# Performance work log

Hardware: AMD Instinct MI355X
Metric: run time of the kernel (lower is better)

## Reference

```python
import jax, jax.numpy as jnp
import numpy as np

N, E = 50000, 1600000
DIM_IN, HEADS, DIM_OUT = 256, 4, 32
NEG_SLOPE = 0.2


def setup_inputs() -> dict:
    key = jax.random.key(0)
    k1, k2, k3, k4, k5, k6 = jax.random.split(key, 6)
    x = jax.random.normal(k1, (N, DIM_IN), dtype=jnp.float32)
    edge_index = jax.random.randint(k2, (2, E), 0, N, dtype=jnp.int64)
    s = 1.0 / np.sqrt(DIM_IN)
    W = jax.random.normal(k3, (DIM_IN, HEADS * DIM_OUT), dtype=jnp.float32) * s
    att_src = jax.random.normal(k4, (HEADS, DIM_OUT), dtype=jnp.float32) * 0.1
    att_dst = jax.random.normal(k5, (HEADS, DIM_OUT), dtype=jnp.float32) * 0.1
    bias = jax.random.normal(k6, (HEADS * DIM_OUT,), dtype=jnp.float32) * 0.01
    return {"x": x, "edge_index": edge_index, "W": W,
            "att_src": att_src, "att_dst": att_dst, "bias": bias}


def reference(x, edge_index, W, att_src, att_dst, bias):
    n = x.shape[0]
    h, c = att_src.shape
    # linear projection, per-head view [N, H, C]
    xp = (x @ W).reshape(n, h, c)
    # per-node attention logits [N, H]
    a_src = jnp.einsum('nhc,hc->nh', xp, att_src)
    a_dst = jnp.einsum('nhc,hc->nh', xp, att_dst)
    # add self loops (PyG default add_self_loops=True)
    loops = jnp.arange(n, dtype=edge_index.dtype)
    src = jnp.concatenate([edge_index[0], loops])  # [E+N]
    dst = jnp.concatenate([edge_index[1], loops])
    # edge attention scores [E+N, H]
    e = jax.nn.leaky_relu(a_src[src] + a_dst[dst], negative_slope=NEG_SLOPE)
    # segment softmax over incoming edges of each dst node
    emax = jax.ops.segment_max(e, dst, num_segments=n)
    ex = jnp.exp(e - emax[dst])
    denom = jax.ops.segment_sum(ex, dst, num_segments=n)
    alpha = ex / denom[dst]  # [E+N, H]
    # weighted scatter-aggregate of src features
    msg = xp[src] * alpha[:, :, None]  # [E+N, H, C]
    out = jax.ops.segment_sum(msg, dst, num_segments=n)  # [N, H, C]
    return out.reshape(n, h * c) + bias
```

## Files before the change

kernel.cpp:

```cpp
#include <hip/hip_runtime.h>
#include <hip/hip_fp16.h>


#define DIN 256
#define HC 128
#define NH 4
#define NEG 0.2f
#define BCAP 12288
#define LOG2E 1.44269504f

typedef _Float16 half8 __attribute__((ext_vector_type(8)));
typedef _Float16 half2v __attribute__((ext_vector_type(2)));
typedef float f32x4 __attribute__((ext_vector_type(4)));

__device__ __forceinline__ void proj_body(char* sm, int tid, const float* __restrict__ x,
                                          const _Float16* __restrict__ Wt,
                                          const float* __restrict__ attS,
                                          const float* __restrict__ attD,
                                          __half* __restrict__ xph,
                                          float* __restrict__ a_src,
                                          float* __restrict__ a_dst, int n, int node0) {
    _Float16* xs = (_Float16*)sm;
    _Float16* Wl = (_Float16*)(sm + 5120);
    _Float16* ep = (_Float16*)sm;
    float* attSL = (float*)(sm + 17408);
    float* attDL = (float*)(sm + 17920);

    const int wave = tid >> 6;
    const int lane = tid & 63;
    const int l15  = lane & 15;
    const int quad = lane >> 4;

    if (tid < 128) attSL[tid] = attS[tid];
    else           attDL[tid - 128] = attD[tid - 128];

    f32x4 acc[8];
#pragma unroll
    for (int ct = 0; ct < 8; ++ct) acc[ct] = (f32x4){0.f, 0.f, 0.f, 0.f};

    for (int kt = 0; kt < DIN; kt += 32) {
        __syncthreads();
#pragma unroll
        for (int r = 0; r < 4; ++r) {
            int idx = tid + r * 256;
            int row = idx >> 4;
            int kp  = idx & 15;
            int gn = node0 + row;
            float2 xv = make_float2(0.f, 0.f);
            if (gn < n) xv = *(const float2*)&x[(size_t)gn * DIN + kt + kp * 2];
            half2v p; p[0] = (_Float16)xv.x; p[1] = (_Float16)xv.y;
            *(half2v*)&xs[row * 40 + kp * 2] = p;
        }
#pragma unroll
        for (int r = 0; r < 2; ++r) {
            int id = tid + r * 256;
            int c = id >> 2;
            int q = id & 3;
            half8 wv = *(const half8*)&Wt[(size_t)c * 256 + kt + q * 8];
            *(half8*)&Wl[c * 40 + q * 8] = wv;
        }
        __syncthreads();
        half8 af = *(const half8*)&xs[(wave * 16 + l15) * 40 + quad * 8];
#pragma unroll
        for (int ct = 0; ct < 8; ++ct) {
            half8 bf = *(const half8*)&Wl[(ct * 16 + l15) * 40 + quad * 8];
            acc[ct] = __builtin_amdgcn_mfma_f32_16x16x32_f16(af, bf, acc[ct], 0, 0, 0);
        }
    }
    __syncthreads();
#pragma unroll
    for (int ct = 0; ct < 8; ++ct)
#pragma unroll
        for (int r = 0; r < 4; ++r) {
            int row = wave * 16 + quad * 4 + r;
            ep[row * 136 + ct * 16 + l15] = (_Float16)acc[ct][r];
        }
    __syncthreads();
    {
        int row = tid >> 2, ch = tid & 3;
        int node = node0 + row;
        if (node < n) {
            const uint4* s = (const uint4*)&ep[row * 136 + ch * 32];
            uint4* d = (uint4*)&xph[(size_t)node * HC + ch * 32];
            d[0] = s[0]; d[1] = s[1]; d[2] = s[2]; d[3] = s[3];
        }
    }
    {
        int nl = tid >> 2, h = tid & 3;
        int node = node0 + nl;
        if (node < n) {
            float ps = 0.f, pd = 0.f;
            const _Float16* er = &ep[nl * 136 + h * 32];
#pragma unroll
            for (int c = 0; c < 32; ++c) {
                float v = (float)er[c];
                ps += v * attSL[h * 32 + c];
                pd += v * attDL[h * 32 + c];
            }
            a_src[node * NH + h] = ps * LOG2E;
            a_dst[node * NH + h] = pd * LOG2E;
        }
    }
}

__global__ __launch_bounds__(256) void k_zero_wtrans(int* __restrict__ gz,
                                                     const float* __restrict__ W,
                                                     _Float16* __restrict__ Wt) {
    const int b = blockIdx.x;
    if (b < 2) {
        gz[b * 256 + threadIdx.x] = 0;
    } else {
        int i = (b - 2) * 256 + threadIdx.x;
        int k = i >> 7, c = i & 127;
        Wt[c * 256 + k] = (_Float16)W[i];
    }
}

__global__ __launch_bounds__(512) void k_bin_proj(const int* __restrict__ ei,
                                                  int* __restrict__ gcur0,
                                                  unsigned* __restrict__ binned,
                                                  const float* __restrict__ x,
                                                  const _Float16* __restrict__ Wt,
                                                  const float* __restrict__ attS,
                                                  const float* __restrict__ attD,
                                                  __half* __restrict__ xph,
                                                  float* __restrict__ a_src,
                                                  float* __restrict__ a_dst,
                                                  int e, int n, int ech) {
    __shared__ __attribute__((aligned(16))) char sm[36864];
    if ((int)blockIdx.x < ech) {
        int* h     = (int*)sm;
        int* rbase = (int*)(sm + 1024);
        const int tid = threadIdx.x;
        if (tid < 256) h[tid] = 0;
        __syncthreads();
        const int base = blockIdx.x * 4096;
        unsigned pk[8];
        int bk[8];
#pragma unroll
        for (int j = 0; j < 8; ++j) {
            int i = base + j * 512 + tid;
            bk[j] = -1;
            if (i < e) {
                int src = ei[i];
                int dst = ei[e + i];
                if ((unsigned)dst < (unsigned)n && (unsigned)src < (unsigned)n) {
                    bk[j] = dst >> 8;
                    pk[j] = ((unsigned)(dst & 255) << 16) | (unsigned)src;
                    atomicAdd(&h[bk[j]], 1);
                }
            }
        }
        __syncthreads();
        if (tid < 256) {
            if (h[tid]) rbase[tid] = atomicAdd(&gcur0[tid], h[tid]);
            h[tid] = 0;
        }
        __syncthreads();
#pragma unroll
        for (int j = 0; j < 8; ++j) {
            if (bk[j] >= 0) {
                int p = atomicAdd(&h[bk[j]], 1);
                int pib = rbase[bk[j]] + p;
                if (pib < BCAP) binned[(size_t)bk[j] * BCAP + pib] = pk[j];
            }
        }
    } else {
        const int sub = threadIdx.x >> 8;
        const int tid = threadIdx.x & 255;
        const int tile = ((int)blockIdx.x - ech) * 2 + sub;
        proj_body(sm + sub * 18432, tid, x, Wt, attS, attD, xph, a_src, a_dst, n, tile * 64);
    }
}

__global__ __launch_bounds__(1024) void k_csr(const unsigned* __restrict__ binned,
                                              const int* __restrict__ gcnt,
                                              int* __restrict__ off,
                                              int* __restrict__ deg,
                                              unsigned short* __restrict__ srt,
                                              int n) {
    __shared__ int cnt[256], buf[256], cur[256];
    const int tid = threadIdx.x;
    const int b = blockIdx.x;
    if (tid < 256) { buf[tid] = min(gcnt[tid], BCAP); cnt[tid] = 0; }
    __syncthreads();
    for (int s = 1; s < 256; s <<= 1) {
        int t = (tid < 256 && tid >= s) ? buf[tid - s] : 0;
        __syncthreads();
        if (tid < 256) buf[tid] += t;
        __syncthreads();
    }
    const int cb = min(gcnt[b], BCAP);
    const int excl = buf[b] - cb;
    const int pgbase = ((excl + 31) & ~31) + b * 8192;
    const int kb = b * BCAP;
    const int ke = kb + cb;
    __syncthreads();
    for (int i = kb + tid; i < ke; i += 1024)
        atomicAdd(&cnt[binned[i] >> 16], 1);
    __syncthreads();
    int v = 0;
    if (tid < 256) { v = cnt[tid]; buf[tid] = (v + 31) & ~31; }
    __syncthreads();
    for (int s = 1; s < 256; s <<= 1) {
        int t = (tid < 256 && tid >= s) ? buf[tid - s] : 0;
        __syncthreads();
        if (tid < 256) buf[tid] += t;
        __syncthreads();
    }
    if (tid < 256) {
        const int myoff = pgbase + buf[tid] - ((v + 31) & ~31);
        const int node = b * 256 + tid;
        if (node < n) { off[node] = myoff; deg[node] = v; }
        cur[tid] = myoff;
    }
    __syncthreads();
    for (int i = kb + tid; i < ke; i += 1024) {
        unsigned pv = binned[i];
        int nl = pv >> 16;
        int pos = atomicAdd(&cur[nl], 1);
        srt[pos] = (unsigned short)(pv & 0xFFFFu);
    }
}

__global__ __launch_bounds__(256) void agg_kernel(const __half* __restrict__ xph,
                                                  const float* __restrict__ a_src,
                                                  const float* __restrict__ a_dst,
                                                  const int* __restrict__ off,
                                                  const int* __restrict__ deg,
                                                  const unsigned short* __restrict__ srt,
                                                  const float* __restrict__ bias,
                                                  float* __restrict__ out, int n) {
    const int node = (blockIdx.x * blockDim.x + threadIdx.x) >> 6;
    if (node >= n) return;
    const int lane = threadIdx.x & 63;
    const int g = lane >> 4;
    const unsigned l = (unsigned)(lane & 15);
    const unsigned h = l >> 2;
    const unsigned lo8 = l * 8u;

    const float ad = a_dst[((unsigned)node << 2) + h];

    float acc[8];
#pragma unroll
    for (int c = 0; c < 8; ++c) acc[c] = 0.f;
    float den = 0.f;

    if (g == 0) {
        float t = a_src[((unsigned)node << 2) + h] + ad;
        float s = exp2f(fmaxf(t, NEG * t));
        half8 xv = *(const half8*)&xph[((unsigned)node << 7) + lo8];
#pragma unroll
        for (int c = 0; c < 8; ++c) acc[c] = s * (float)xv[c];
        den = s;
    }

    const int kb = off[node];
    const int ke = kb + deg[node];
    int k0 = kb;
    for (; k0 + 16 <= ke; k0 += 16) {
        const unsigned kg = (unsigned)(k0 + g * 4);
        const ushort4 s4 = *(const ushort4*)&srt[kg];
        unsigned sv[4] = {s4.x, s4.y, s4.z, s4.w};
        float asv[4];
        half8 hv[4];
#pragma unroll
        for (int j = 0; j < 4; ++j) asv[j] = a_src[(sv[j] << 2) + h];
#pragma unroll
        for (int j = 0; j < 4; ++j)
            hv[j] = *(const half8*)&xph[(sv[j] << 7) + lo8];
#pragma unroll
        for (int j = 0; j < 4; ++j) {
            float t = asv[j] + ad;
            const float s = exp2f(fmaxf(t, NEG * t));
#pragma unroll
            for (int c = 0; c < 8; ++c) acc[c] += s * (float)hv[j][c];
            den += s;
        }
    }
    if (k0 < ke) {
        const unsigned kg = (unsigned)(k0 + g * 4);
        const ushort4 s4 = *(const ushort4*)&srt[kg];
        const unsigned sv[4] = {s4.x, s4.y, s4.z, s4.w};
#pragma unroll
        for (int j = 0; j < 4; ++j) {
            if ((int)kg + j < ke) {
                float t = a_src[(sv[j] << 2) + h] + ad;
                const float s = exp2f(fmaxf(t, NEG * t));
                const half8 hv = *(const half8*)&xph[(sv[j] << 7) + lo8];
#pragma unroll
                for (int c = 0; c < 8; ++c) acc[c] += s * (float)hv[c];
                den += s;
            }
        }
    }

#pragma unroll
    for (int c = 0; c < 8; ++c) acc[c] += __shfl_xor(acc[c], 16, 64);
    den += __shfl_xor(den, 16, 64);
#pragma unroll
    for (int c = 0; c < 8; ++c) acc[c] += __shfl_xor(acc[c], 32, 64);
    den += __shfl_xor(den, 32, 64);

    if (lane < 16) {
        const float inv = 1.0f / den;
        const float4* b4 = (const float4*)&bias[lo8];
        float4 o0, o1;
        o0.x = acc[0] * inv + b4[0].x;
        o0.y = acc[1] * inv + b4[0].y;
        o0.z = acc[2] * inv + b4[0].z;
        o0.w = acc[3] * inv + b4[0].w;
        o1.x = acc[4] * inv + b4[1].x;
        o1.y = acc[5] * inv + b4[1].y;
        o1.z = acc[6] * inv + b4[1].z;
        o1.w = acc[7] * inv + b4[1].w;
        float4* d = (float4*)&out[((unsigned)node << 7) + lo8];
        d[0] = o0;
        d[1] = o1;
    }
}

extern "C" void kernel_launch(void* const* d_in, const int* in_sizes, int n_in,
                              void* d_out, int out_size, void* d_ws, size_t ws_size,
                              hipStream_t stream) {
    if (n_in < 6 || !d_out || !d_ws) return;
    const float* x    = (const float*)d_in[0];
    const int*   ei   = (const int*)d_in[1];
    const float* W    = (const float*)d_in[2];
    const float* attS = (const float*)d_in[3];
    const float* attD = (const float*)d_in[4];
    const float* bias = (const float*)d_in[5];
    float* out = (float*)d_out;

    const int N = in_sizes[0] / DIN;
    const int E = in_sizes[1] / 2;
    if (N <= 0 || E <= 0) return;
    const int NBUCK = (N + 255) >> 8;
    if (NBUCK > 256 || N > 65536) return;

    char* ws = (char*)d_ws;
    size_t off_b = 0;
    auto carve = [&](size_t bytes) {
        size_t p = off_b;
        off_b = (off_b + bytes + 255) & ~(size_t)255;
        return (void*)(ws + p);
    };
    __half*         xph    = (__half*)carve((size_t)N * HC * 2);
    _Float16*       Wt     = (_Float16*)carve((size_t)HC * DIN * 2);
    float*          a_src  = (float*)carve((size_t)N * NH * 4);
    float*          a_dst  = (float*)carve((size_t)N * NH * 4);
    int*            gz     = (int*)carve(512 * 4);
    unsigned*       binned = (unsigned*)carve((size_t)NBUCK * BCAP * 4);
    int*            offp   = (int*)carve((size_t)N * 4);
    int*            degp   = (int*)carve((size_t)N * 4);
    unsigned short* srt    = (unsigned short*)carve(((size_t)E + (size_t)NBUCK * 8192 + 64) * 2);
    (void)out_size;
    if (off_b > ws_size) return;

    int* gcur0 = gz;

    const int ECH = (E + 4095) / 4096;
    const int PB  = (N + 63) / 64;
    const int PBH = (PB + 1) / 2;

    k_zero_wtrans<<<2 + 128, 256, 0, stream>>>(gz, W, Wt);
    k_bin_proj<<<ECH + PBH, 512, 0, stream>>>(ei, gcur0, binned, x, Wt, attS, attD,
                                              xph, a_src, a_dst, E, N, ECH);
    k_csr<<<NBUCK, 1024, 0, stream>>>(binned, gcur0, offp, degp, srt, N);
    agg_kernel<<<(N * 64 + 255) / 256, 256, 0, stream>>>(xph, a_src, a_dst,
                                                         offp, degp, srt, bias, out, N);
}
```

Baseline: 217.1 us.

## Fuse weight transpose, binning, projection and CSR into one flag-synchronized kernel

Merges the zero/transpose, bin+projection and CSR-build kernels into a single persistent-style launch. Block roles are chosen by block index, and global atomic flags with acquire/release spin-waits enforce the dependencies: the projection waits for the weight transpose and the CSR role waits for all binning blocks. This removes two kernel launch boundaries and lets independent roles overlap. It relies on every block being co-resident or scheduled in index order to avoid deadlock, and adds a grid-size guard plus a memset for the counters. The aggregation kernel also makes the node index wave-uniform with readfirstlane.

New measurement: 572.4 us. 164% more time.

```diff
diff --git a/kernel.cpp b/kernel.cpp
--- a/kernel.cpp
+++ b/kernel.cpp
@@ -103,85 +103,56 @@
     }
 }
 
-__global__ __launch_bounds__(256) void k_zero_wtrans(int* __restrict__ gz,
-                                                     const float* __restrict__ W,
-                                                     _Float16* __restrict__ Wt) {
-    const int b = blockIdx.x;
-    if (b < 2) {
-        gz[b * 256 + threadIdx.x] = 0;
-    } else {
-        int i = (b - 2) * 256 + threadIdx.x;
-        int k = i >> 7, c = i & 127;
-        Wt[c * 256 + k] = (_Float16)W[i];
-    }
-}
-
-__global__ __launch_bounds__(512) void k_bin_proj(const int* __restrict__ ei,
-                                                  int* __restrict__ gcur0,
-                                                  unsigned* __restrict__ binned,
-                                                  const float* __restrict__ x,
-                                                  const _Float16* __restrict__ Wt,
-                                                  const float* __restrict__ attS,
-                                                  const float* __restrict__ attD,
-                                                  __half* __restrict__ xph,
-                                                  float* __restrict__ a_src,
-                                                  float* __restrict__ a_dst,
-                                                  int e, int n, int ech) {
-    __shared__ __attribute__((aligned(16))) char sm[36864];
-    if ((int)blockIdx.x < ech) {
-        int* h     = (int*)sm;
-        int* rbase = (int*)(sm + 1024);
-        const int tid = threadIdx.x;
-        if (tid < 256) h[tid] = 0;
-        __syncthreads();
-        const int base = blockIdx.x * 4096;
-        unsigned pk[8];
-        int bk[8];
-#pragma unroll
-        for (int j = 0; j < 8; ++j) {
-            int i = base + j * 512 + tid;
-            bk[j] = -1;
-            if (i < e) {
-                int src = ei[i];
-                int dst = ei[e + i];
-                if ((unsigned)dst < (unsigned)n && (unsigned)src < (unsigned)n) {
-                    bk[j] = dst >> 8;
-                    pk[j] = ((unsigned)(dst & 255) << 16) | (unsigned)src;
-                    atomicAdd(&h[bk[j]], 1);
-                }
+__device__ __forceinline__ void bin_role(char* sm, const int* __restrict__ ei,
+                                         int* __restrict__ gcur0,
+                                         unsigned* __restrict__ binned,
+                                         int e, int n, int chunk) {
+    int* h     = (int*)sm;
+    int* rbase = (int*)(sm + 1024);
+    const int tid = threadIdx.x;
+    if (tid < 256) h[tid] = 0;
+    __syncthreads();
+    const int base = chunk * 4096;
+    unsigned pk[8];
+    int bk[8];
+#pragma unroll
+    for (int j = 0; j < 8; ++j) {
+        int i = base + j * 512 + tid;
+        bk[j] = -1;
+        if (i < e) {
+            int src = ei[i];
+            int dst = ei[e + i];
+            if ((unsigned)dst < (unsigned)n && (unsigned)src < (unsigned)n) {
+                bk[j] = dst >> 8;
+                pk[j] = ((unsigned)(dst & 255) << 16) | (unsigned)src;
+                atomicAdd(&h[bk[j]], 1);
             }
         }
-        __syncthreads();
-        if (tid < 256) {
-            if (h[tid]) rbase[tid] = atomicAdd(&gcur0[tid], h[tid]);
-            h[tid] = 0;
-        }
-        __syncthreads();
-#pragma unroll
-        for (int j = 0; j < 8; ++j) {
-            if (bk[j] >= 0) {
-                int p = atomicAdd(&h[bk[j]], 1);
-                int pib = rbase[bk[j]] + p;
-                if (pib < BCAP) binned[(size_t)bk[j] * BCAP + pib] = pk[j];
-            }
-        }
-    } else {
-        const int sub = threadIdx.x >> 8;
-        const int tid = threadIdx.x & 255;
-        const int tile = ((int)blockIdx.x - ech) * 2 + sub;
-        proj_body(sm + sub * 18432, tid, x, Wt, attS, attD, xph, a_src, a_dst, n, tile * 64);
-    }
-}
-
-__global__ __launch_bounds__(1024) void k_csr(const unsigned* __restrict__ binned,
-                                              const int* __restrict__ gcnt,
-                                              int* __restrict__ off,
-                                              int* __restrict__ deg,
-                                              unsigned short* __restrict__ srt,
-                                              int n) {
-    __shared__ int cnt[256], buf[256], cur[256];
+    }
+    __syncthreads();
+    if (tid < 256) {
+        if (h[tid]) rbase[tid] = atomicAdd(&gcur0[tid], h[tid]);
+        h[tid] = 0;
+    }
+    __syncthreads();
+#pragma unroll
+    for (int j = 0; j < 8; ++j) {
+        if (bk[j] >= 0) {
+            int p = atomicAdd(&h[bk[j]], 1);
+            int pib = rbase[bk[j]] + p;
+            if (pib < BCAP) binned[(size_t)bk[j] * BCAP + pib] = pk[j];
+        }
+    }
+}
+
+__device__ __forceinline__ void csr_role(char* sm, const unsigned* __restrict__ binned,
+                                         const int* __restrict__ gcnt,
+                                         int* __restrict__ off, int* __restrict__ deg,
+                                         unsigned short* __restrict__ srt, int n, int b) {
+    int* cnt = (int*)sm;
+    int* buf = (int*)(sm + 1024);
+    int* cur = (int*)(sm + 2048);
     const int tid = threadIdx.x;
-    const int b = blockIdx.x;
     if (tid < 256) { buf[tid] = min(gcnt[tid], BCAP); cnt[tid] = 0; }
     __syncthreads();
     for (int s = 1; s < 256; s <<= 1) {
@@ -196,7 +167,7 @@
     const int kb = b * BCAP;
     const int ke = kb + cb;
     __syncthreads();
-    for (int i = kb + tid; i < ke; i += 1024)
+    for (int i = kb + tid; i < ke; i += 512)
         atomicAdd(&cnt[binned[i] >> 16], 1);
     __syncthreads();
     int v = 0;
@@ -215,11 +186,68 @@
         cur[tid] = myoff;
     }
     __syncthreads();
-    for (int i = kb + tid; i < ke; i += 1024) {
+    for (int i = kb + tid; i < ke; i += 512) {
         unsigned pv = binned[i];
         int nl = pv >> 16;
         int pos = atomicAdd(&cur[nl], 1);
         srt[pos] = (unsigned short)(pv & 0xFFFFu);
+    }
+}
+
+__global__ __launch_bounds__(512, 8) void k_mega(const int* __restrict__ ei,
+                                                 int* __restrict__ gcur0,
+                                                 int* __restrict__ flags,
+                                                 unsigned* __restrict__ binned,
+                                                 const float* __restrict__ x,
+                                                 const float* __restrict__ W,
+                                                 _Float16* __restrict__ Wt,
+                                                 const float* __restrict__ attS,
+                                                 const float* __restrict__ attD,
+                                                 __half* __restrict__ xph,
+                                                 float* __restrict__ a_src,
+                                                 float* __restrict__ a_dst,
+                                                 int* __restrict__ off,
+                                                 int* __restrict__ deg,
+                                                 unsigned short* __restrict__ srt,
+                                                 int e, int n, int ech, int pbh, int nbuck) {
+    __shared__ __attribute__((aligned(16))) char sm[36864];
+    const int bid = blockIdx.x;
+    const int tid = threadIdx.x;
+
+    if (bid < ech) {
+        if (bid < 64) {
+            int idx = bid * 512 + tid;
+            int k = idx >> 7, c = idx & 127;
+            Wt[c * 256 + k] = (_Float16)W[idx];
+            __threadfence();
+            __syncthreads();
+            if (tid == 0)
+                __hip_atomic_fetch_add(&flags[0], 1, __ATOMIC_RELEASE, __HIP_MEMORY_SCOPE_AGENT);
+        }
+        bin_role(sm, ei, gcur0, binned, e, n, bid);
+        __threadfence();
+        __syncthreads();
+        if (tid == 0)
+            __hip_atomic_fetch_add(&flags[1], 1, __ATOMIC_RELEASE, __HIP_MEMORY_SCOPE_AGENT);
+    } else if (bid < ech + pbh) {
+        if (tid == 0) {
+            while (__hip_atomic_load(&flags[0], __ATOMIC_ACQUIRE, __HIP_MEMORY_SCOPE_AGENT) < 64)
+                __builtin_amdgcn_s_sleep(32);
+        }
+        __syncthreads();
+        __threadfence();
+        const int sub = tid >> 8;
+        const int t2  = tid & 255;
+        const int tile = (bid - ech) * 2 + sub;
+        proj_body(sm + sub * 18432, t2, x, Wt, attS, attD, xph, a_src, a_dst, n, tile * 64);
+    } else {
+        if (tid == 0) {
+            while (__hip_atomic_load(&flags[1], __ATOMIC_ACQUIRE, __HIP_MEMORY_SCOPE_AGENT) < ech)
+                __builtin_amdgcn_s_sleep(32);
+        }
+        __syncthreads();
+        __threadfence();
+        csr_role(sm, binned, gcur0, off, deg, srt, n, bid - ech - pbh);
     }
 }
 
@@ -231,8 +259,9 @@
                                                   const unsigned short* __restrict__ srt,
                                                   const float* __restrict__ bias,
                                                   float* __restrict__ out, int n) {
-    const int node = (blockIdx.x * blockDim.x + threadIdx.x) >> 6;
-    if (node >= n) return;
+    int node_ = (blockIdx.x * blockDim.x + threadIdx.x) >> 6;
+    if (node_ >= n) return;
+    const int node = __builtin_amdgcn_readfirstlane(node_);
     const int lane = threadIdx.x & 63;
     const int g = lane >> 4;
     const unsigned l = (unsigned)(lane & 15);
@@ -336,7 +365,10 @@
     const int E = in_sizes[1] / 2;
     if (N <= 0 || E <= 0) return;
     const int NBUCK = (N + 255) >> 8;
-    if (NBUCK > 256 || N > 65536) return;
+    const int ECH = (E + 4095) / 4096;
+    const int PB  = (N + 63) / 64;
+    const int PBH = (PB + 1) / 2;
+    if (NBUCK > 256 || N > 65536 || ECH < 64 || ECH + PBH + NBUCK > 1000) return;
 
     char* ws = (char*)d_ws;
     size_t off_b = 0;
@@ -358,15 +390,12 @@
     if (off_b > ws_size) return;
 
     int* gcur0 = gz;
-
-    const int ECH = (E + 4095) / 4096;
-    const int PB  = (N + 63) / 64;
-    const int PBH = (PB + 1) / 2;
-
-    k_zero_wtrans<<<2 + 128, 256, 0, stream>>>(gz, W, Wt);
-    k_bin_proj<<<ECH + PBH, 512, 0, stream>>>(ei, gcur0, binned, x, Wt, attS, attD,
-                                              xph, a_src, a_dst, E, N, ECH);
-    k_csr<<<NBUCK, 1024, 0, stream>>>(binned, gcur0, offp, degp, srt, N);
+    int* flags = gz + 256;
+
+    hipMemsetAsync(gz, 0, 2048, stream);
+    k_mega<<<ECH + PBH + NBUCK, 512, 0, stream>>>(ei, gcur0, flags, binned, x, W, Wt,
+                                                  attS, attD, xph, a_src, a_dst,
+                                                  offp, degp, srt, E, N, ECH, PBH, NBUCK);
     agg_kernel<<<(N * 64 + 255) / 256, 256, 0, stream>>>(xph, a_src, a_dst,
                                                          offp, degp, srt, bias, out, N);
 }
```
